# Optimization experiments

Measured on AMD Instinct MI355X. Metric: run time of the kernel, lower is better.

The kernel has to match this reference:

```python
import jax, jax.numpy as jnp
import numpy as np

N_NODES = 100000
D_IN = 128
D_HID = 128
N_EDGES = 1600000


def setup_inputs() -> dict:
    key = jax.random.key(0)
    ks = jax.random.split(key, 8)
    x = jax.random.normal(ks[0], (N_NODES, D_IN), dtype=jnp.float32)
    edge_index = jax.random.randint(ks[1], (2, N_EDGES), 0, N_NODES, dtype=jnp.int64)
    s = 1.0 / np.sqrt(D_IN)
    W1l = jax.random.uniform(ks[2], (D_IN, D_HID), jnp.float32, -s, s)
    W1r = jax.random.uniform(ks[3], (D_IN, D_HID), jnp.float32, -s, s)
    b1 = jnp.zeros((D_HID,), jnp.float32)
    sh = 1.0 / np.sqrt(D_HID)
    W2l = jax.random.uniform(ks[4], (D_HID, D_HID), jnp.float32, -sh, sh)
    W2r = jax.random.uniform(ks[5], (D_HID, D_HID), jnp.float32, -sh, sh)
    b2 = jnp.zeros((D_HID,), jnp.float32)
    return {"x": x, "edge_index": edge_index, "W1l": W1l, "W1r": W1r,
            "b1": b1, "W2l": W2l, "W2r": W2r, "b2": b2}


def _sage_conv(x, src, dst, Wl, Wr, b, n_nodes):
    # mean-aggregate neighbor features: gather x[src], scatter-add at dst
    msgs = x[src]                                                  # [E, D]
    agg = jax.ops.segment_sum(msgs, dst, num_segments=n_nodes)    # [N, D]
    cnt = jax.ops.segment_sum(jnp.ones((src.shape[0],), x.dtype), dst,
                              num_segments=n_nodes)               # [N]
    agg = agg / jnp.maximum(cnt, 1.0)[:, None]
    # SAGEConv: lin_l(aggregated) + lin_r(root) + bias
    return agg @ Wl + x @ Wr + b


def reference(x, edge_index, W1l, W1r, b1, W2l, W2r, b2):
    src, dst = edge_index[0], edge_index[1]
    n = x.shape[0]
    h = jax.nn.relu(_sage_conv(x, src, dst, W1l, W1r, b1, n))
    return _sage_conv(h, src, dst, W2l, W2r, b2, n)
```

## Files before the change

kernel.cpp:

```cpp
#include <hip/hip_runtime.h>

#define D 128
constexpr int TILE_ROWS  = 64;
constexpr int BUCKET_CAP = 2048;
constexpr int LISTS_CAP  = 2304;
constexpr int LDS_STRIDE = 136;

constexpr int SB_SHIFT   = 11;
constexpr int SB_MASK    = (1 << SB_SHIFT) - 1;
constexpr int MAX_NSB    = 52;
constexpr int SB_CAP     = 40960;
constexpr int CNT_STRIDE = 32;
constexpr int P1_CHUNK   = 4096;
constexpr int P1_CAP     = 192;
constexpr int P2_CHUNK   = 4096;
constexpr int P2_KBLK    = 12;
constexpr int P2_CAP     = 192;

using bf16x8 = __attribute__((ext_vector_type(8))) short;
using f32x4  = __attribute__((ext_vector_type(4))) float;
typedef float f32x2_t __attribute__((ext_vector_type(2)));

static __device__ __forceinline__ unsigned short f2bf(float f) {
    unsigned int u = __float_as_uint(f);
    unsigned int r = (u + 0x7FFFu + ((u >> 16) & 1u)) >> 16;
    return (unsigned short)r;
}

__global__ __launch_bounds__(256)
void bin_pass1(const int* __restrict__ src, const int* __restrict__ dst,
               int* __restrict__ gcnt, int* __restrict__ sbent, int E, int nsb) {
    __shared__ int fifo[MAX_NSB][P1_CAP];
    __shared__ int fcnt[MAX_NSB];

    const int tid  = threadIdx.x;
    const int base = blockIdx.x * P1_CHUNK;

    for (int i = tid; i < nsb; i += 256) fcnt[i] = 0;
    __syncthreads();

    int ds[16], ss[16];
    #pragma unroll
    for (int q = 0; q < 16; ++q) {
        const int e = base + q * 256 + tid;
        const bool v = e < E;
        ds[q] = v ? dst[e] : -1;
        ss[q] = v ? src[e] : 0;
    }
    #pragma unroll
    for (int q = 0; q < 16; ++q) {
        if (ds[q] < 0) continue;
        const int sb = ds[q] >> SB_SHIFT;
        const int entry = (ss[q] << SB_SHIFT) | (ds[q] & SB_MASK);
        const int pos = atomicAdd(&fcnt[sb], 1);
        if (pos < P1_CAP) {
            fifo[sb][pos] = entry;
        } else {
            const int gp = atomicAdd(&gcnt[sb * CNT_STRIDE], 1);
            if (gp < SB_CAP) sbent[(size_t)sb * SB_CAP + gp] = entry;
        }
    }
    __syncthreads();

    const int wid = tid >> 6, lane = tid & 63;
    for (int sb = wid; sb < nsb; sb += 4) {
        int n = fcnt[sb];
        if (n > P1_CAP) n = P1_CAP;
        if (n == 0) continue;
        int gbase;
        if (lane == 0) gbase = atomicAdd(&gcnt[sb * CNT_STRIDE], n);
        gbase = __shfl(gbase, 0, 64);
        for (int i = lane; i < n; i += 64)
            if (gbase + i < SB_CAP)
                sbent[(size_t)sb * SB_CAP + gbase + i] = fifo[sb][i];
    }
}

__global__ __launch_bounds__(256)
void bin_pass2(const int* __restrict__ gcnt, const int* __restrict__ sbent,
               int* __restrict__ tcnt, int* __restrict__ buckets) {
    __shared__ int fifo[32][P2_CAP];
    __shared__ int fcnt[32];

    const int sb = blockIdx.x / P2_KBLK;
    const int c  = blockIdx.x % P2_KBLK;
    const int n  = min(gcnt[sb * CNT_STRIDE], SB_CAP);
    const int beg = c * P2_CHUNK;
    const int end = min(beg + P2_CHUNK, n);
    if (beg >= end) return;

    const int tid = threadIdx.x;
    if (tid < 32) fcnt[tid] = 0;
    __syncthreads();

    for (int i = beg + tid; i < end; i += 256) {
        const int entry = sbent[(size_t)sb * SB_CAP + i];
        const int dl = entry & SB_MASK;
        const int t  = dl >> 6;
        const int out = ((entry >> SB_SHIFT) << 6) | (dl & 63);
        const int pos = atomicAdd(&fcnt[t], 1);
        if (pos < P2_CAP) {
            fifo[t][pos] = out;
        } else {
            const int tile = sb * 32 + t;
            const int gp = atomicAdd(&tcnt[tile], 1);
            if (gp < BUCKET_CAP) buckets[(size_t)tile * BUCKET_CAP + gp] = out;
        }
    }
    __syncthreads();

    const int wid = tid >> 6, lane = tid & 63;
    for (int t = wid; t < 32; t += 4) {
        int n2 = fcnt[t];
        if (n2 > P2_CAP) n2 = P2_CAP;
        if (n2 == 0) continue;
        const int tile = sb * 32 + t;
        int gbase;
        if (lane == 0) gbase = atomicAdd(&tcnt[tile], n2);
        gbase = __shfl(gbase, 0, 64);
        for (int i = lane; i < n2; i += 64)
            if (gbase + i < BUCKET_CAP)
                buckets[(size_t)tile * BUCKET_CAP + gbase + i] = fifo[t][i];
    }
}

__global__ void cast_x(const float* __restrict__ x, unsigned short* __restrict__ xb,
                       unsigned int* __restrict__ xf8, int n4) {
    int i = blockIdx.x * blockDim.x + threadIdx.x;
    if (i >= n4) return;
    const float4 v = *(const float4*)(x + (size_t)i * 4);
    ushort4 o;
    o.x = f2bf(v.x); o.y = f2bf(v.y); o.z = f2bf(v.z); o.w = f2bf(v.w);
    *(ushort4*)(xb + (size_t)i * 4) = o;
    int p = __builtin_amdgcn_cvt_pk_fp8_f32(v.x, v.y, 0, false);
    p     = __builtin_amdgcn_cvt_pk_fp8_f32(v.z, v.w, p, true);
    xf8[i] = (unsigned int)p;
}

__global__ void wswz_kernel(const float* __restrict__ W1l, const float* __restrict__ W1r,
                            const float* __restrict__ W2l, const float* __restrict__ W2r,
                            unsigned short* __restrict__ Wsw) {
    int idx = blockIdx.x * blockDim.x + threadIdx.x;
    if (idx >= 2 * 8 * 8 * 64 * 8) return;
    const int j  = idx & 7;
    const int l  = (idx >> 3) & 63;
    const int t  = (idx >> 9) & 7;
    const int kc = (idx >> 12) & 7;
    const int L  = idx >> 15;
    const int k  = (kc & 3) * 32 + 8 * (l >> 4) + j;
    const int n  = t * 16 + (l & 15);
    const float* W = L ? ((kc < 4) ? W2l : W2r) : ((kc < 4) ? W1l : W1r);
    Wsw[idx] = f2bf(W[k * D + n]);
}

template <bool RELU, bool BF16OUT, bool F8OUT>
__global__ __launch_bounds__(256)
void sage_layer(const unsigned short* __restrict__ Xb,
                const unsigned int* __restrict__ Xf8,
                const int* __restrict__ tcnt,
                const int* __restrict__ buckets,
                const unsigned short* __restrict__ Wsw,
                const float* __restrict__ bias,
                void* __restrict__ outv,
                unsigned char* __restrict__ outf8,
                int N) {
    __shared__ unsigned short sAgg[TILE_ROWS * LDS_STRIDE];
    __shared__ __align__(16) int lists[LISTS_CAP];
    __shared__ int cnt64[TILE_ROWS], off64[TILE_ROWS], cur64[TILE_ROWS];

    const int tid = threadIdx.x;
    const int b   = blockIdx.x;
    const int rowBase = b * TILE_ROWS;

    const int nE = min(tcnt[b], BUCKET_CAP);
    const int* myb = buckets + (size_t)b * BUCKET_CAP;
    int ent[8];
    #pragma unroll
    for (int q = 0; q < 8; ++q) {
        const int i = tid + q * 256;
        ent[q] = (i < nE) ? myb[i] : -1;
    }
    if (tid < 64) { cnt64[tid] = 0; cur64[tid] = 0; }
    __syncthreads();
    #pragma unroll
    for (int q = 0; q < 8; ++q)
        if (ent[q] >= 0) atomicAdd(&cnt64[ent[q] & 63], 1);
    __syncthreads();
    if (tid < 64) {
        const int v  = cnt64[tid];
        const int rv = (v + 3) & ~3;
        int incl = rv;
        #pragma unroll
        for (int o = 1; o < 64; o <<= 1) {
            const int t = __shfl_up(incl, o, 64);
            if (tid >= o) incl += t;
        }
        off64[tid] = incl - rv;
    }
    __syncthreads();
    #pragma unroll
    for (int q = 0; q < 8; ++q)
        if (ent[q] >= 0) {
            const int d = ent[q] & 63;
            lists[off64[d] + atomicAdd(&cur64[d], 1)] = ent[q] >> 6;
        }
    __syncthreads();

    const int wid  = tid >> 6;
    const int lane = tid & 63;
    const int half = lane >> 5;
    const int c4   = lane & 31;

    for (int g = 0; g < 4; ++g) {
        int dg[4], bs[4];
        int nbmax = 0;
        #pragma unroll
        for (int n = 0; n < 4; ++n) {
            const int ld = wid * 16 + g * 4 + n;
            dg[n] = cnt64[ld];
            bs[n] = off64[ld];
            nbmax = max(nbmax, (dg[n] + 15) >> 4);
        }
        f32x2_t s01[4], s23[4];
        #pragma unroll
        for (int n = 0; n < 4; ++n) { s01[n] = 0.f; s23[n] = 0.f; }

        for (int bb = 0; bb < nbmax; ++bb) {
            const int ebase = bb * 16 + half * 8;
            unsigned int u[4][8];
            #pragma unroll
            for (int n = 0; n < 4; ++n) {
                const int4 ia = *(const int4*)&lists[bs[n] + ebase];
                const int4 ib = *(const int4*)&lists[bs[n] + ebase + 4];
                const int idxs[8] = {ia.x, ia.y, ia.z, ia.w, ib.x, ib.y, ib.z, ib.w};
                const int d = dg[n];
                #pragma unroll
                for (int q = 0; q < 8; ++q) {
                    unsigned int v = 0;
                    if (ebase + q < d)
                        v = Xf8[(size_t)idxs[q] * 32 + c4];
                    u[n][q] = v;
                }
            }
            #pragma unroll
            for (int n = 0; n < 4; ++n) {
                #pragma unroll
                for (int q = 0; q < 8; ++q) {
                    s01[n] += __builtin_amdgcn_cvt_pk_f32_fp8((int)u[n][q], false);
                    s23[n] += __builtin_amdgcn_cvt_pk_f32_fp8((int)u[n][q], true);
                }
            }
        }

        #pragma unroll
        for (int n = 0; n < 4; ++n) {
            float a0 = s01[n][0], a1 = s01[n][1], a2 = s23[n][0], a3 = s23[n][1];
            a0 += __shfl_xor(a0, 32, 64);
            a1 += __shfl_xor(a1, 32, 64);
            a2 += __shfl_xor(a2, 32, 64);
            a3 += __shfl_xor(a3, 32, 64);
            const int deg = dg[n];
            const float rd = (deg > 0) ? 1.0f / (float)deg : 0.f;
            if (lane < 32) {
                const unsigned int w0 = (unsigned int)f2bf(a0 * rd) |
                                        ((unsigned int)f2bf(a1 * rd) << 16);
                const unsigned int w1 = (unsigned int)f2bf(a2 * rd) |
                                        ((unsigned int)f2bf(a3 * rd) << 16);
                unsigned int* p = (unsigned int*)&sAgg[(wid * 16 + g * 4 + n) * LDS_STRIDE + c4 * 4];
                p[0] = w0; p[1] = w1;
            }
        }
    }
    __syncthreads();

    const int r16  = lane & 15;
    const int koff = (lane >> 4) * 8;
    int arow = rowBase + wid * 16 + r16;
    if (arow >= N) arow = N - 1;
    const unsigned short* Wp = Wsw + lane * 8;

    f32x4 acc[8] = {};
    #pragma unroll
    for (int kc = 0; kc < 8; ++kc) {
        const int k0 = (kc & 3) * 32;
        bf16x8 afrag;
        if (kc < 4)
            afrag = *(const bf16x8*)(&sAgg[(wid * 16 + r16) * LDS_STRIDE + k0 + koff]);
        else
            afrag = *(const bf16x8*)(Xb + (size_t)arow * D + k0 + koff);
        #pragma unroll
        for (int t = 0; t < 8; ++t) {
            const bf16x8 bfrag = *(const bf16x8*)(Wp + (size_t)(kc * 8 + t) * 512);
            acc[t] = __builtin_amdgcn_mfma_f32_16x16x32_bf16(afrag, bfrag, acc[t], 0, 0, 0);
        }
    }

    const int mBase = rowBase + wid * 16 + 4 * (lane >> 4);
    const int nSub  = lane & 15;
    #pragma unroll
    for (int t = 0; t < 8; ++t) {
        const int n = t * 16 + nSub;
        const float bv = bias[n];
        #pragma unroll
        for (int r = 0; r < 4; ++r) {
            const int m = mBase + r;
            if (m < N) {
                float v = acc[t][r] + bv;
                if (RELU) v = fmaxf(v, 0.f);
                if (BF16OUT)
                    ((unsigned short*)outv)[(size_t)m * D + n] = f2bf(v);
                else
                    ((float*)outv)[(size_t)m * D + n] = v;
                if (F8OUT) {
                    const int pk = __builtin_amdgcn_cvt_pk_fp8_f32(v, 0.f, 0, false);
                    outf8[(size_t)m * D + n] = (unsigned char)(pk & 0xFF);
                }
            }
        }
    }
}

extern "C" void kernel_launch(void* const* d_in, const int* in_sizes, int n_in,
                              void* d_out, int out_size, void* d_ws, size_t ws_size,
                              hipStream_t stream) {
    const float* x   = (const float*)d_in[0];
    const int*  edge = (const int*)d_in[1];
    const float* W1l = (const float*)d_in[2];
    const float* W1r = (const float*)d_in[3];
    const float* b1  = (const float*)d_in[4];
    const float* W2l = (const float*)d_in[5];
    const float* W2r = (const float*)d_in[6];
    const float* b2  = (const float*)d_in[7];
    float* out = (float*)d_out;

    const int N = in_sizes[0] / D;
    const int E = in_sizes[1] / 2;
    const int* src = edge;
    const int* dst = edge + E;
    const int nbuckets = (N + TILE_ROWS - 1) / TILE_ROWS;
    const int nsb = (N + (1 << SB_SHIFT) - 1) >> SB_SHIFT;

    char* ws = (char*)d_ws;
    auto alignup = [](size_t v) { return (v + 255) & ~(size_t)255; };
    int* gcnt    = (int*)ws;             ws += alignup((size_t)MAX_NSB * CNT_STRIDE * 4);
    int* tcnt    = (int*)ws;             ws += alignup((size_t)nbuckets * 4);
    int* sbent   = (int*)ws;             ws += alignup((size_t)MAX_NSB * SB_CAP * 4);
    int* buckets = (int*)ws;             ws += alignup((size_t)nbuckets * BUCKET_CAP * 4);
    unsigned short* xb  = (unsigned short*)ws;  ws += alignup((size_t)N * D * 2);
    unsigned int*   xf8 = (unsigned int*)ws;    ws += alignup((size_t)N * D);
    unsigned short* hb  = (unsigned short*)ws;  ws += alignup((size_t)N * D * 2);
    unsigned char*  hf8 = (unsigned char*)ws;   ws += alignup((size_t)N * D);
    unsigned short* Wsw = (unsigned short*)ws;  ws += alignup((size_t)65536 * 2);

    hipMemsetAsync(gcnt, 0, (size_t)MAX_NSB * CNT_STRIDE * 4, stream);
    hipMemsetAsync(tcnt, 0, (size_t)nbuckets * 4, stream);

    const int n4 = N * D / 4;
    cast_x<<<(n4 + 255) / 256, 256, 0, stream>>>(x, xb, xf8, n4);
    wswz_kernel<<<65536 / 256, 256, 0, stream>>>(W1l, W1r, W2l, W2r, Wsw);

    bin_pass1<<<(E + P1_CHUNK - 1) / P1_CHUNK, 256, 0, stream>>>(src, dst, gcnt, sbent, E, nsb);
    bin_pass2<<<nsb * P2_KBLK, 256, 0, stream>>>(gcnt, sbent, tcnt, buckets);

    sage_layer<true, true, true><<<nbuckets, 256, 0, stream>>>(
        xb, xf8, tcnt, buckets, Wsw, b1, hb, hf8, N);
    sage_layer<false, false, false><<<nbuckets, 256, 0, stream>>>(
        hb, (const unsigned int*)hf8, tcnt, buckets, Wsw + 32768, b2, out, nullptr, N);
}
```

Before: 204.3 us.

## Double block size to 512 threads and pad neighbor lists with zero sentinel row

Each sage_layer block now runs 512 threads (8 waves). Each wave aggregates 8 destination rows instead of 16, and in the GEMM phase each wave computes half of the output columns for a 16-row strip. Per-row neighbor lists are padded to multiples of 16 with a sentinel index pointing to an extra zeroed fp8 row, so the per-element bounds check in the gather loop is replaced by one per-block check. The aim is more memory-level parallelism in the gather and fewer branches. The cost is larger LDS lists, higher register pressure limits, and extra sentinel loads.

```diff
diff --git a/kernel.cpp b/kernel.cpp
--- a/kernel.cpp
+++ b/kernel.cpp
@@ -3,7 +3,7 @@
 #define D 128
 constexpr int TILE_ROWS  = 64;
 constexpr int BUCKET_CAP = 2048;
-constexpr int LISTS_CAP  = 2304;
+constexpr int LISTS_CAP  = 3072;
 constexpr int LDS_STRIDE = 136;
 
 constexpr int SB_SHIFT   = 11;
@@ -154,7 +154,7 @@
 }
 
 template <bool RELU, bool BF16OUT, bool F8OUT>
-__global__ __launch_bounds__(256)
+__global__ __launch_bounds__(512)
 void sage_layer(const unsigned short* __restrict__ Xb,
                 const unsigned int* __restrict__ Xf8,
                 const int* __restrict__ tcnt,
@@ -174,21 +174,21 @@
 
     const int nE = min(tcnt[b], BUCKET_CAP);
     const int* myb = buckets + (size_t)b * BUCKET_CAP;
-    int ent[8];
-    #pragma unroll
-    for (int q = 0; q < 8; ++q) {
-        const int i = tid + q * 256;
+    int ent[4];
+    #pragma unroll
+    for (int q = 0; q < 4; ++q) {
+        const int i = tid + q * 512;
         ent[q] = (i < nE) ? myb[i] : -1;
     }
     if (tid < 64) { cnt64[tid] = 0; cur64[tid] = 0; }
     __syncthreads();
     #pragma unroll
-    for (int q = 0; q < 8; ++q)
+    for (int q = 0; q < 4; ++q)
         if (ent[q] >= 0) atomicAdd(&cnt64[ent[q] & 63], 1);
     __syncthreads();
     if (tid < 64) {
         const int v  = cnt64[tid];
-        const int rv = (v + 3) & ~3;
+        const int rv = (v + 15) & ~15;
         int incl = rv;
         #pragma unroll
         for (int o = 1; o < 64; o <<= 1) {
@@ -199,11 +199,17 @@
     }
     __syncthreads();
     #pragma unroll
-    for (int q = 0; q < 8; ++q)
+    for (int q = 0; q < 4; ++q)
         if (ent[q] >= 0) {
             const int d = ent[q] & 63;
             lists[off64[d] + atomicAdd(&cur64[d], 1)] = ent[q] >> 6;
         }
+    if (tid < 64) {
+        const int d0  = cnt64[tid];
+        const int d1  = (d0 + 15) & ~15;
+        const int off = off64[tid];
+        for (int i = d0; i < d1; ++i) lists[off + i] = N;
+    }
     __syncthreads();
 
     const int wid  = tid >> 6;
@@ -211,15 +217,16 @@
     const int half = lane >> 5;
     const int c4   = lane & 31;
 
-    for (int g = 0; g < 4; ++g) {
-        int dg[4], bs[4];
+    for (int g = 0; g < 2; ++g) {
+        int dg[4], bs[4], nb[4];
         int nbmax = 0;
         #pragma unroll
         for (int n = 0; n < 4; ++n) {
-            const int ld = wid * 16 + g * 4 + n;
+            const int ld = wid * 8 + g * 4 + n;
             dg[n] = cnt64[ld];
             bs[n] = off64[ld];
-            nbmax = max(nbmax, (dg[n] + 15) >> 4);
+            nb[n] = (dg[n] + 15) >> 4;
+            nbmax = max(nbmax, nb[n]);
         }
         f32x2_t s01[4], s23[4];
         #pragma unroll
@@ -230,16 +237,16 @@
             unsigned int u[4][8];
             #pragma unroll
             for (int n = 0; n < 4; ++n) {
-                const int4 ia = *(const int4*)&lists[bs[n] + ebase];
-                const int4 ib = *(const int4*)&lists[bs[n] + ebase + 4];
-                const int idxs[8] = {ia.x, ia.y, ia.z, ia.w, ib.x, ib.y, ib.z, ib.w};
-                const int d = dg[n];
-                #pragma unroll
-                for (int q = 0; q < 8; ++q) {
-                    unsigned int v = 0;
-                    if (ebase + q < d)
-                        v = Xf8[(size_t)idxs[q] * 32 + c4];
-                    u[n][q] = v;
+                if (bb < nb[n]) {
+                    const int4 ia = *(const int4*)&lists[bs[n] + ebase];
+                    const int4 ib = *(const int4*)&lists[bs[n] + ebase + 4];
+                    const int idxs[8] = {ia.x, ia.y, ia.z, ia.w, ib.x, ib.y, ib.z, ib.w};
+                    #pragma unroll
+                    for (int q = 0; q < 8; ++q)
+                        u[n][q] = Xf8[(size_t)idxs[q] * 32 + c4];
+                } else {
+                    #pragma unroll
+                    for (int q = 0; q < 8; ++q) u[n][q] = 0;
                 }
             }
             #pragma unroll
@@ -266,7 +273,7 @@
                                         ((unsigned int)f2bf(a1 * rd) << 16);
                 const unsigned int w1 = (unsigned int)f2bf(a2 * rd) |
                                         ((unsigned int)f2bf(a3 * rd) << 16);
-                unsigned int* p = (unsigned int*)&sAgg[(wid * 16 + g * 4 + n) * LDS_STRIDE + c4 * 4];
+                unsigned int* p = (unsigned int*)&sAgg[(wid * 8 + g * 4 + n) * LDS_STRIDE + c4 * 4];
                 p[0] = w0; p[1] = w1;
             }
         }
@@ -275,31 +282,34 @@
 
     const int r16  = lane & 15;
     const int koff = (lane >> 4) * 8;
-    int arow = rowBase + wid * 16 + r16;
+    const int wrow = (wid & 3) * 16;
+    const int ch   = wid >> 2;
+    int arow = rowBase + wrow + r16;
     if (arow >= N) arow = N - 1;
     const unsigned short* Wp = Wsw + lane * 8;
 
-    f32x4 acc[8] = {};
+    f32x4 acc[4] = {};
     #pragma unroll
     for (int kc = 0; kc < 8; ++kc) {
         const int k0 = (kc & 3) * 32;
         bf16x8 afrag;
         if (kc < 4)
-            afrag = *(const bf16x8*)(&sAgg[(wid * 16 + r16) * LDS_STRIDE + k0 + koff]);
+            afrag = *(const bf16x8*)(&sAgg[(wrow + r16) * LDS_STRIDE + k0 + koff]);
         else
             afrag = *(const bf16x8*)(Xb + (size_t)arow * D + k0 + koff);
         #pragma unroll
-        for (int t = 0; t < 8; ++t) {
-            const bf16x8 bfrag = *(const bf16x8*)(Wp + (size_t)(kc * 8 + t) * 512);
+        for (int t = 0; t < 4; ++t) {
+            const int tp = ch * 4 + t;
+            const bf16x8 bfrag = *(const bf16x8*)(Wp + (size_t)(kc * 8 + tp) * 512);
             acc[t] = __builtin_amdgcn_mfma_f32_16x16x32_bf16(afrag, bfrag, acc[t], 0, 0, 0);
         }
     }
 
-    const int mBase = rowBase + wid * 16 + 4 * (lane >> 4);
+    const int mBase = rowBase + wrow + 4 * (lane >> 4);
     const int nSub  = lane & 15;
     #pragma unroll
-    for (int t = 0; t < 8; ++t) {
-        const int n = t * 16 + nSub;
+    for (int t = 0; t < 4; ++t) {
+        const int n = (ch * 4 + t) * 16 + nSub;
         const float bv = bias[n];
         #pragma unroll
         for (int r = 0; r < 4; ++r) {
@@ -347,13 +357,15 @@
     int* sbent   = (int*)ws;             ws += alignup((size_t)MAX_NSB * SB_CAP * 4);
     int* buckets = (int*)ws;             ws += alignup((size_t)nbuckets * BUCKET_CAP * 4);
     unsigned short* xb  = (unsigned short*)ws;  ws += alignup((size_t)N * D * 2);
-    unsigned int*   xf8 = (unsigned int*)ws;    ws += alignup((size_t)N * D);
+    unsigned int*   xf8 = (unsigned int*)ws;    ws += alignup((size_t)(N + 1) * D);
     unsigned short* hb  = (unsigned short*)ws;  ws += alignup((size_t)N * D * 2);
-    unsigned char*  hf8 = (unsigned char*)ws;   ws += alignup((size_t)N * D);
+    unsigned char*  hf8 = (unsigned char*)ws;   ws += alignup((size_t)(N + 1) * D);
     unsigned short* Wsw = (unsigned short*)ws;  ws += alignup((size_t)65536 * 2);
 
     hipMemsetAsync(gcnt, 0, (size_t)MAX_NSB * CNT_STRIDE * 4, stream);
     hipMemsetAsync(tcnt, 0, (size_t)nbuckets * 4, stream);
+    hipMemsetAsync(xf8 + (size_t)N * 32, 0, D, stream);
+    hipMemsetAsync(hf8 + (size_t)N * D,  0, D, stream);
 
     const int n4 = N * D / 4;
     cast_x<<<(n4 + 255) / 256, 256, 0, stream>>>(x, xb, xf8, n4);
@@ -362,8 +374,8 @@
     bin_pass1<<<(E + P1_CHUNK - 1) / P1_CHUNK, 256, 0, stream>>>(src, dst, gcnt, sbent, E, nsb);
     bin_pass2<<<nsb * P2_KBLK, 256, 0, stream>>>(gcnt, sbent, tcnt, buckets);
 
-    sage_layer<true, true, true><<<nbuckets, 256, 0, stream>>>(
+    sage_layer<true, true, true><<<nbuckets, 512, 0, stream>>>(
         xb, xf8, tcnt, buckets, Wsw, b1, hb, hf8, N);
-    sage_layer<false, false, false><<<nbuckets, 256, 0, stream>>>(
+    sage_layer<false, false, false><<<nbuckets, 512, 0, stream>>>(
         hb, (const unsigned int*)hf8, tcnt, buckets, Wsw + 32768, b2, out, nullptr, N);
 }
```

After: 209.3 us. 1.02x slower.

## Build per-tile CSR once in a separate pass and reuse it across both layers

Applied to the files above, without the earlier changes.

Adds a csr_pass kernel that sorts each tile's bucketed edges into per-node neighbour lists, padded to multiples of 16 with a dummy zero row (index N). The result is written to global memory once. Both sage_layer launches now read these precomputed lists instead of each rebuilding them in LDS, which removes duplicated sorting work and shrinks LDS use in the layer kernel. The padding also drops the per-edge bounds check in the gather loop. The cost is an extra kernel launch and an extra global round trip for the CSR lists.

```diff
diff --git a/kernel.cpp b/kernel.cpp
--- a/kernel.cpp
+++ b/kernel.cpp
@@ -3,7 +3,7 @@
 #define D 128
 constexpr int TILE_ROWS  = 64;
 constexpr int BUCKET_CAP = 2048;
-constexpr int LISTS_CAP  = 2304;
+constexpr int LISTS_CAP  = 3072;
 constexpr int LDS_STRIDE = 136;
 
 constexpr int SB_SHIFT   = 11;
@@ -122,6 +122,63 @@
             if (gbase + i < BUCKET_CAP)
                 buckets[(size_t)tile * BUCKET_CAP + gbase + i] = fifo[t][i];
     }
+}
+
+__global__ __launch_bounds__(256)
+void csr_pass(const int* __restrict__ tcnt, const int* __restrict__ buckets,
+              int* __restrict__ node_cnt, int* __restrict__ node_off,
+              int* __restrict__ gcsr, int N) {
+    __shared__ __align__(16) int lists[LISTS_CAP];
+    __shared__ int cnt64[64], off64[64], cur64[64], s_tot[1];
+
+    const int tid = threadIdx.x;
+    const int b   = blockIdx.x;
+
+    const int nE = min(tcnt[b], BUCKET_CAP);
+    const int* myb = buckets + (size_t)b * BUCKET_CAP;
+    int ent[8];
+    #pragma unroll
+    for (int q = 0; q < 8; ++q) {
+        const int i = tid + q * 256;
+        ent[q] = (i < nE) ? myb[i] : -1;
+    }
+    if (tid < 64) { cnt64[tid] = 0; cur64[tid] = 0; }
+    __syncthreads();
+    #pragma unroll
+    for (int q = 0; q < 8; ++q)
+        if (ent[q] >= 0) atomicAdd(&cnt64[ent[q] & 63], 1);
+    __syncthreads();
+    if (tid < 64) {
+        const int v  = cnt64[tid];
+        const int rv = (v + 15) & ~15;
+        int incl = rv;
+        #pragma unroll
+        for (int o = 1; o < 64; o <<= 1) {
+            const int t = __shfl_up(incl, o, 64);
+            if (tid >= o) incl += t;
+        }
+        off64[tid] = incl - rv;
+        if (tid == 63) s_tot[0] = incl;
+    }
+    __syncthreads();
+    #pragma unroll
+    for (int q = 0; q < 8; ++q)
+        if (ent[q] >= 0) {
+            const int d = ent[q] & 63;
+            lists[off64[d] + atomicAdd(&cur64[d], 1)] = ent[q] >> 6;
+        }
+    if (tid < 64) {
+        const int d0  = cnt64[tid];
+        const int d1  = (d0 + 15) & ~15;
+        const int off = off64[tid];
+        for (int i = d0; i < d1; ++i) lists[off + i] = N;
+        node_cnt[b * 64 + tid] = d0;
+        node_off[b * 64 + tid] = b * LISTS_CAP + off;
+    }
+    __syncthreads();
+    const int tot = s_tot[0];
+    for (int i = tid; i < tot; i += 256)
+        gcsr[(size_t)b * LISTS_CAP + i] = lists[i];
 }
 
 __global__ void cast_x(const float* __restrict__ x, unsigned short* __restrict__ xb,
@@ -157,54 +214,19 @@
 __global__ __launch_bounds__(256)
 void sage_layer(const unsigned short* __restrict__ Xb,
                 const unsigned int* __restrict__ Xf8,
-                const int* __restrict__ tcnt,
-                const int* __restrict__ buckets,
+                const int* __restrict__ node_cnt,
+                const int* __restrict__ node_off,
+                const int* __restrict__ gcsr,
                 const unsigned short* __restrict__ Wsw,
                 const float* __restrict__ bias,
                 void* __restrict__ outv,
                 unsigned char* __restrict__ outf8,
                 int N) {
     __shared__ unsigned short sAgg[TILE_ROWS * LDS_STRIDE];
-    __shared__ __align__(16) int lists[LISTS_CAP];
-    __shared__ int cnt64[TILE_ROWS], off64[TILE_ROWS], cur64[TILE_ROWS];
 
     const int tid = threadIdx.x;
     const int b   = blockIdx.x;
     const int rowBase = b * TILE_ROWS;
-
-    const int nE = min(tcnt[b], BUCKET_CAP);
-    const int* myb = buckets + (size_t)b * BUCKET_CAP;
-    int ent[8];
-    #pragma unroll
-    for (int q = 0; q < 8; ++q) {
-        const int i = tid + q * 256;
-        ent[q] = (i < nE) ? myb[i] : -1;
-    }
-    if (tid < 64) { cnt64[tid] = 0; cur64[tid] = 0; }
-    __syncthreads();
-    #pragma unroll
-    for (int q = 0; q < 8; ++q)
-        if (ent[q] >= 0) atomicAdd(&cnt64[ent[q] & 63], 1);
-    __syncthreads();
-    if (tid < 64) {
-        const int v  = cnt64[tid];
-        const int rv = (v + 3) & ~3;
-        int incl = rv;
-        #pragma unroll
-        for (int o = 1; o < 64; o <<= 1) {
-            const int t = __shfl_up(incl, o, 64);
-            if (tid >= o) incl += t;
-        }
-        off64[tid] = incl - rv;
-    }
-    __syncthreads();
-    #pragma unroll
-    for (int q = 0; q < 8; ++q)
-        if (ent[q] >= 0) {
-            const int d = ent[q] & 63;
-            lists[off64[d] + atomicAdd(&cur64[d], 1)] = ent[q] >> 6;
-        }
-    __syncthreads();
 
     const int wid  = tid >> 6;
     const int lane = tid & 63;
@@ -212,14 +234,15 @@
     const int c4   = lane & 31;
 
     for (int g = 0; g < 4; ++g) {
-        int dg[4], bs[4];
+        int dg[4], bs[4], nb[4];
         int nbmax = 0;
         #pragma unroll
         for (int n = 0; n < 4; ++n) {
-            const int ld = wid * 16 + g * 4 + n;
-            dg[n] = cnt64[ld];
-            bs[n] = off64[ld];
-            nbmax = max(nbmax, (dg[n] + 15) >> 4);
+            const int node = rowBase + wid * 16 + g * 4 + n;
+            dg[n] = node_cnt[node];
+            bs[n] = node_off[node];
+            nb[n] = (dg[n] + 15) >> 4;
+            nbmax = max(nbmax, nb[n]);
         }
         f32x2_t s01[4], s23[4];
         #pragma unroll
@@ -230,16 +253,16 @@
             unsigned int u[4][8];
             #pragma unroll
             for (int n = 0; n < 4; ++n) {
-                const int4 ia = *(const int4*)&lists[bs[n] + ebase];
-                const int4 ib = *(const int4*)&lists[bs[n] + ebase + 4];
-                const int idxs[8] = {ia.x, ia.y, ia.z, ia.w, ib.x, ib.y, ib.z, ib.w};
-                const int d = dg[n];
-                #pragma unroll
-                for (int q = 0; q < 8; ++q) {
-                    unsigned int v = 0;
-                    if (ebase + q < d)
-                        v = Xf8[(size_t)idxs[q] * 32 + c4];
-                    u[n][q] = v;
+                if (bb < nb[n]) {
+                    const int4 ia = *(const int4*)&gcsr[bs[n] + ebase];
+                    const int4 ib = *(const int4*)&gcsr[bs[n] + ebase + 4];
+                    const int idxs[8] = {ia.x, ia.y, ia.z, ia.w, ib.x, ib.y, ib.z, ib.w};
+                    #pragma unroll
+                    for (int q = 0; q < 8; ++q)
+                        u[n][q] = Xf8[(size_t)idxs[q] * 32 + c4];
+                } else {
+                    #pragma unroll
+                    for (int q = 0; q < 8; ++q) u[n][q] = 0;
                 }
             }
             #pragma unroll
@@ -342,18 +365,23 @@
 
     char* ws = (char*)d_ws;
     auto alignup = [](size_t v) { return (v + 255) & ~(size_t)255; };
-    int* gcnt    = (int*)ws;             ws += alignup((size_t)MAX_NSB * CNT_STRIDE * 4);
-    int* tcnt    = (int*)ws;             ws += alignup((size_t)nbuckets * 4);
-    int* sbent   = (int*)ws;             ws += alignup((size_t)MAX_NSB * SB_CAP * 4);
-    int* buckets = (int*)ws;             ws += alignup((size_t)nbuckets * BUCKET_CAP * 4);
+    int* gcnt     = (int*)ws;            ws += alignup((size_t)MAX_NSB * CNT_STRIDE * 4);
+    int* tcnt     = (int*)ws;            ws += alignup((size_t)nbuckets * 4);
+    int* sbent    = (int*)ws;            ws += alignup((size_t)MAX_NSB * SB_CAP * 4);
+    int* buckets  = (int*)ws;            ws += alignup((size_t)nbuckets * BUCKET_CAP * 4);
+    int* gcsr     = (int*)ws;            ws += alignup((size_t)nbuckets * LISTS_CAP * 4);
+    int* node_cnt = (int*)ws;            ws += alignup((size_t)nbuckets * 64 * 4);
+    int* node_off = (int*)ws;            ws += alignup((size_t)nbuckets * 64 * 4);
     unsigned short* xb  = (unsigned short*)ws;  ws += alignup((size_t)N * D * 2);
-    unsigned int*   xf8 = (unsigned int*)ws;    ws += alignup((size_t)N * D);
+    unsigned int*   xf8 = (unsigned int*)ws;    ws += alignup((size_t)(N + 1) * D);
     unsigned short* hb  = (unsigned short*)ws;  ws += alignup((size_t)N * D * 2);
-    unsigned char*  hf8 = (unsigned char*)ws;   ws += alignup((size_t)N * D);
+    unsigned char*  hf8 = (unsigned char*)ws;   ws += alignup((size_t)(N + 1) * D);
     unsigned short* Wsw = (unsigned short*)ws;  ws += alignup((size_t)65536 * 2);
 
     hipMemsetAsync(gcnt, 0, (size_t)MAX_NSB * CNT_STRIDE * 4, stream);
     hipMemsetAsync(tcnt, 0, (size_t)nbuckets * 4, stream);
+    hipMemsetAsync(xf8 + (size_t)N * 32, 0, D, stream);
+    hipMemsetAsync(hf8 + (size_t)N * D,  0, D, stream);
 
     const int n4 = N * D / 4;
     cast_x<<<(n4 + 255) / 256, 256, 0, stream>>>(x, xb, xf8, n4);
@@ -361,9 +389,10 @@
 
     bin_pass1<<<(E + P1_CHUNK - 1) / P1_CHUNK, 256, 0, stream>>>(src, dst, gcnt, sbent, E, nsb);
     bin_pass2<<<nsb * P2_KBLK, 256, 0, stream>>>(gcnt, sbent, tcnt, buckets);
+    csr_pass<<<nbuckets, 256, 0, stream>>>(tcnt, buckets, node_cnt, node_off, gcsr, N);
 
     sage_layer<true, true, true><<<nbuckets, 256, 0, stream>>>(
-        xb, xf8, tcnt, buckets, Wsw, b1, hb, hf8, N);
+        xb, xf8, node_cnt, node_off, gcsr, Wsw, b1, hb, hf8, N);
     sage_layer<false, false, false><<<nbuckets, 256, 0, stream>>>(
-        hb, (const unsigned int*)hf8, tcnt, buckets, Wsw + 32768, b2, out, nullptr, N);
-}
+        hb, (const unsigned int*)hf8, node_cnt, node_off, gcsr, Wsw + 32768, b2, out, nullptr, N);
+}
```

Result: slower. 256.0 us (+25.3%).
